# Performance work log

Measured on AMD Instinct MI355X. Metric: run time of the kernel, lower is better.

The kernel has to match this reference:

```python
import jax, jax.numpy as jnp
import numpy as np

N = 6000; E = 96000; DIN = 3000; FH1 = 256; FH2 = 128; GH = 128; LAT = 256
K = 10; SCALE = 9; NC = 10; AT = 0.5; ALPHA = 1.0; BN_EPS = 1e-4

# eval-mode BatchNorm1d with running_mean=0, running_var=1
def _bn(x, g, b):
    return x * (g / jnp.sqrt(1.0 + BN_EPS)) + b

def _block(x, W, bb, g, be):  # Linear + BN(eval) + ELU (dropout=identity in eval)
    return jax.nn.elu(_bn(x @ W + bb, g, be))

def _tconv(x, src, dst, Wq, Wk, Wv, Ws, bq, bk, bv, bs):
    # PyG TransformerConv, heads=1, root_weight=True, eval (no dropout)
    q = x @ Wq + bq; k = x @ Wk + bk; v = x @ Wv + bv
    sc = 1.0 / jnp.sqrt(jnp.asarray(q.shape[-1], x.dtype))
    logit = jnp.sum(q[dst] * k[src], axis=-1) * sc            # [E]
    m = jax.ops.segment_max(logit, dst, num_segments=N)
    e = jnp.exp(logit - m[dst])
    s = jax.ops.segment_sum(e, dst, num_segments=N)
    alpha = e / s[dst]                                        # softmax over incoming edges
    out = jax.ops.segment_sum(alpha[:, None] * v[src], dst, num_segments=N) + x @ Ws + bs
    return out, alpha

def _dense_adj(src, dst, alpha):
    # remove_self_loops + to_dense_adj: dense[src, dst] += alpha for src != dst
    mask = (src != dst).astype(alpha.dtype)
    return jnp.zeros((N, N), alpha.dtype).at[src, dst].add(alpha * mask)

def _encode(x, adj, adjp, ew1, eb1, eg1, ebe1, ew2, eb2, eg2, ebe2,
            cWq, cWk, cWv, cWs, cbq, cbk, cbv, cbs):
    feat = _block(_block(x, ew1, eb1, eg1, ebe1), ew2, eb2, eg2, ebe2)
    h = feat
    lastAp = None
    for l in range(3):
        o, a = _tconv(h, adj[0], adj[1], cWq[l], cWk[l], cWv[l], cWs[l], cbq[l], cbk[l], cbv[l], cbs[l])
        # middle layer applies the 'prue' conv to the freshly produced x (as in source)
        hp_in = o if l == 1 else h
        op, ap = _tconv(hp_in, adjp[0], adjp[1], cWq[l], cWk[l], cWv[l], cWs[l], cbq[l], cbk[l], cbv[l], cbs[l])
        A = _dense_adj(adj[0], adj[1], a)
        Ap = _dense_adj(adjp[0], adjp[1], ap)
        h = (1.0 - AT) * (A @ o) + AT * (Ap @ op)
        if l < 2:
            h = jax.nn.relu(h)
        lastAp = Ap
    return h, feat, lastAp

def setup_inputs():
    key = jax.random.key(0)
    ks = jax.random.split(key, 24)
    w = lambda k, sh, fan: (jax.random.normal(k, sh, jnp.float32) / np.sqrt(fan)).astype(jnp.float32)
    inp = {}
    inp['x'] = jax.random.normal(ks[0], (N, DIN), jnp.float32)
    inp['x_neighbor'] = jax.random.normal(ks[1], (N, DIN), jnp.float32)
    inp['spatial'] = jax.random.uniform(ks[2], (N, 2), jnp.float32)
    inp['adj'] = jax.random.randint(ks[3], (2, E), 0, N, dtype=jnp.int32)
    inp['adj_prue'] = jax.random.randint(ks[4], (2, E), 0, N, dtype=jnp.int32)
    # encoder
    inp['enc_W1'] = w(ks[5], (DIN, FH1), DIN); inp['enc_b1'] = jnp.zeros((FH1,))
    inp['enc_g1'] = jnp.ones((FH1,)); inp['enc_be1'] = jnp.zeros((FH1,))
    inp['enc_W2'] = w(ks[6], (FH1, FH2), FH1); inp['enc_b2'] = jnp.zeros((FH2,))
    inp['enc_g2'] = jnp.ones((FH2,)); inp['enc_be2'] = jnp.zeros((FH2,))
    # 3 TransformerConv layers (gc1, conv_hidden[0], gc2) all 128->128: stacked
    inp['conv_Wq'] = w(ks[7], (3, GH, GH), GH); inp['conv_Wk'] = w(ks[8], (3, GH, GH), GH)
    inp['conv_Wv'] = w(ks[9], (3, GH, GH), GH); inp['conv_Ws'] = w(ks[10], (3, GH, GH), GH)
    inp['conv_bq'] = jnp.zeros((3, GH)); inp['conv_bk'] = jnp.zeros((3, GH))
    inp['conv_bv'] = jnp.zeros((3, GH)); inp['conv_bs'] = jnp.zeros((3, GH))
    # decoder
    inp['dec_W'] = w(ks[11], (LAT, DIN), LAT); inp['dec_b'] = jnp.zeros((DIN,))
    inp['dec_g'] = jnp.ones((DIN,)); inp['dec_be'] = jnp.zeros((DIN,))
    inp['cluster'] = w(ks[12], (NC, LAT), LAT)
    return inp

def reference(x, x_neighbor, spatial, enc_W1, enc_b1, enc_g1, enc_be1,
              enc_W2, enc_b2, enc_g2, enc_be2,
              conv_Wq, conv_Wk, conv_Wv, conv_Ws, conv_bq, conv_bk, conv_bv, conv_bs,
              dec_W, dec_b, dec_g, dec_be, cluster, adj, adj_prue):
    enc = (enc_W1, enc_b1, enc_g1, enc_be1, enc_W2, enc_b2, enc_g2, enc_be2)
    conv = (conv_Wq, conv_Wk, conv_Wv, conv_Ws, conv_bq, conv_bk, conv_bv, conv_bs)
    mu, feat_x, atten = _encode(x, adj, adj_prue, *enc, *conv)
    mu_nb, feat_nb, _ = _encode(x_neighbor, adj, adj_prue, *enc, *conv)
    z = jnp.concatenate([feat_x, mu], axis=1)          # [N, LAT]
    z_nb = jnp.concatenate([feat_nb, mu_nb], axis=1)
    # Graph_spatial: kNN in joint feature+spatial space (dense [N,N] distances)
    df = (jnp.sum(z * z, 1)[:, None] - 2.0 * (z @ z_nb.T) + jnp.sum(z_nb * z_nb, 1)[None, :])
    ds = (jnp.sum(spatial * spatial, 1)[:, None] - 2.0 * (spatial @ spatial.T)
          + jnp.sum(spatial * spatial, 1)[None, :])
    neg_top, idx_k = jax.lax.top_k(-(df + ds), K)      # [N, K]
    score_k = jax.nn.softmax(neg_top, axis=-1)
    # GCNBlock_spatial: gather scale=9 nearest neighbor features and aggregate
    idx9 = idx_k[:, :SCALE]
    x_h = z_nb[idx9]                                   # [N, 9, LAT]
    wgt = score_k[:, :SCALE]
    wgt = wgt / jnp.sum(wgt, axis=-1, keepdims=True)
    z_out = z + jnp.einsum('nk,nkd->nd', wgt, x_h)     # x1_lr
    x1_hr = (x_h * wgt[:, :, None]).reshape(N * SCALE, LAT)
    de_feat = _block(z_out, dec_W, dec_b, dec_g, dec_be)
    # student-t cluster assignment
    d2 = jnp.sum((z_out[:, None, :] - cluster[None, :, :]) ** 2, axis=2)
    q = (1.0 / (1.0 + d2 / ALPHA)) ** ((ALPHA + 1.0) / 2.0)
    q = q / jnp.sum(q, axis=1, keepdims=True)
    return (z_out, de_feat, q, feat_x, de_feat, x1_hr, atten)
```

## Files before the change

kernel.cpp:

```cpp
#include <hip/hip_runtime.h>
#include <hip/hip_bf16.h>
#include <math.h>
#include <stdint.h>

#define NN 6000
#define NE 96000
#define KDIN 3000
#define NCAND 12
#define NTILE 47
#define TCAND (NCAND*NTILE)
#define PRE 32

#define OFF_ZOUT 0
#define OFF_DE1  1536000
#define OFF_Q    19536000
#define OFF_FEAT 19596000
#define OFF_DE2  20364000
#define OFF_X1   38364000
#define OFF_ATT  52188000

typedef __attribute__((ext_vector_type(8))) short short8;
typedef __attribute__((ext_vector_type(4))) float f32x4;

__device__ __forceinline__ unsigned short f2bf(float f){
  unsigned int u = __float_as_uint(f);
  u += 0x7FFFu + ((u >> 16) & 1u);
  return (unsigned short)(u >> 16);
}
__device__ __forceinline__ float bf2f(unsigned short h){
  return __uint_as_float(((unsigned int)h) << 16);
}

__global__ void prep_k(const float* __restrict__ W1, const float* __restrict__ W2,
                       const float* __restrict__ Wq, const float* __restrict__ Wk,
                       const float* __restrict__ Wv, const float* __restrict__ Ws,
                       const float* __restrict__ bq, const float* __restrict__ bk,
                       const float* __restrict__ bv, const float* __restrict__ bs,
                       const float* __restrict__ decW, const float* __restrict__ spat,
                       double* __restrict__ W1t, double* __restrict__ W2t,
                       double* __restrict__ Bct, float* __restrict__ Dt,
                       double* __restrict__ bcat,
                       double* __restrict__ sx64, double* __restrict__ sy64,
                       double* __restrict__ ssq64,
                       float* __restrict__ sx32, float* __restrict__ sy32)
{
  int t = blockIdx.x * 256 + threadIdx.x;
  if (t < 768000){
    int n = t / 3000, k = t % 3000;
    W1t[t] = (double)W1[(size_t)k * 256 + n]; return;
  }
  t -= 768000;
  if (t < 32768){
    int n = t / 256, k = t % 256;
    W2t[t] = (double)W2[(size_t)k * 128 + n]; return;
  }
  t -= 32768;
  if (t < 196608){
    int l = t / 65536; int rem = t % 65536;
    int n = rem / 128, k = rem % 128;
    int sel = n >> 7, nn = n & 127;
    const float* Wm = sel==0 ? Wq : sel==1 ? Wk : sel==2 ? Wv : Ws;
    Bct[t] = (double)Wm[((size_t)(l*128) + k) * 128 + nn]; return;
  }
  t -= 196608;
  if (t < 768000){
    int n = t / 256, k = t % 256;
    Dt[t] = decW[(size_t)k * 3000 + n]; return;
  }
  t -= 768000;
  if (t < 1536){
    int l = t / 512, n = t % 512;
    int sel = n >> 7, nn = n & 127;
    const float* bm = sel==0 ? bq : sel==1 ? bk : sel==2 ? bv : bs;
    bcat[t] = (double)bm[l*128 + nn]; return;
  }
  t -= 1536;
  if (t < NN){
    float sx = spat[(size_t)t*2], sy = spat[(size_t)t*2+1];
    sx64[t]=(double)sx; sy64[t]=(double)sy;
    ssq64[t]=(double)sx*(double)sx + (double)sy*(double)sy;
    sx32[t]=sx; sy32[t]=sy; return;
  }
}

__global__ void castup_k(const float* __restrict__ s, double* __restrict__ d, int n){
  int t = blockIdx.x*256 + threadIdx.x;
  if (t < n) d[t] = (double)s[t];
}

__global__ void splitz_k(const double* __restrict__ z64, unsigned short* __restrict__ zh,
                         unsigned short* __restrict__ zl, int n){
  int t = blockIdx.x*256 + threadIdx.x;
  if (t < n){
    float v = (float)z64[t];
    unsigned short h = f2bf(v);
    float r = v - bf2f(h);
    zh[t] = h; zl[t] = f2bf(r);
  }
}

template<int EPI, typename TA>
__global__ __launch_bounds__(256)
void gemm64_k(const TA* __restrict__ A, int lda,
              const double* __restrict__ Bt, int ldb,
              int M, int K, int Ncol,
              double* __restrict__ outF, int ldc,
              const double* __restrict__ bias,
              const float* __restrict__ gam, const float* __restrict__ bet,
              double* __restrict__ outF2)
{
  __shared__ double lA[64][18];
  __shared__ double lB[64][18];
  const int tid = threadIdx.x;
  const int m0 = blockIdx.y * 64;
  const int n0 = blockIdx.x * 64;
  const int tx = tid & 15;
  const int ty = tid >> 4;

  double acc[4][4];
  #pragma unroll
  for (int i=0;i<4;i++)
    #pragma unroll
    for (int j=0;j<4;j++) acc[i][j] = 0.0;

  const int nkt = (K + 15) >> 4;
  for (int kt = 0; kt < nkt; kt++){
    const int k0 = kt << 4;
    __syncthreads();
    #pragma unroll
    for (int c=0;c<4;c++){
      int lin = tid + c*256;
      int row = lin >> 4, col = lin & 15;
      int gm = m0 + row, gk = k0 + col;
      double va = 0.0, vb = 0.0;
      if (gm < M && gk < K)        va = (double)A [(size_t)gm*lda + gk];
      if (n0+row < Ncol && gk < K) vb = Bt[(size_t)(n0+row)*ldb + gk];
      lA[row][col] = va;
      lB[row][col] = vb;
    }
    __syncthreads();
    #pragma unroll 4
    for (int kk=0; kk<16; kk+=2){
      double2 A0 = *(const double2*)&lA[ty   ][kk];
      double2 A1 = *(const double2*)&lA[ty+16][kk];
      double2 A2 = *(const double2*)&lA[ty+32][kk];
      double2 A3 = *(const double2*)&lA[ty+48][kk];
      double2 B0 = *(const double2*)&lB[tx   ][kk];
      double2 B1 = *(const double2*)&lB[tx+16][kk];
      double2 B2 = *(const double2*)&lB[tx+32][kk];
      double2 B3 = *(const double2*)&lB[tx+48][kk];
      acc[0][0]+=A0.x*B0.x; acc[0][1]+=A0.x*B1.x; acc[0][2]+=A0.x*B2.x; acc[0][3]+=A0.x*B3.x;
      acc[1][0]+=A1.x*B0.x; acc[1][1]+=A1.x*B1.x; acc[1][2]+=A1.x*B2.x; acc[1][3]+=A1.x*B3.x;
      acc[2][0]+=A2.x*B0.x; acc[2][1]+=A2.x*B1.x; acc[2][2]+=A2.x*B2.x; acc[2][3]+=A2.x*B3.x;
      acc[3][0]+=A3.x*B0.x; acc[3][1]+=A3.x*B1.x; acc[3][2]+=A3.x*B2.x; acc[3][3]+=A3.x*B3.x;
      acc[0][0]+=A0.y*B0.y; acc[0][1]+=A0.y*B1.y; acc[0][2]+=A0.y*B2.y; acc[0][3]+=A0.y*B3.y;
      acc[1][0]+=A1.y*B0.y; acc[1][1]+=A1.y*B1.y; acc[1][2]+=A1.y*B2.y; acc[1][3]+=A1.y*B3.y;
      acc[2][0]+=A2.y*B0.y; acc[2][1]+=A2.y*B1.y; acc[2][2]+=A2.y*B2.y; acc[2][3]+=A2.y*B3.y;
      acc[3][0]+=A3.y*B0.y; acc[3][1]+=A3.y*B1.y; acc[3][2]+=A3.y*B2.y; acc[3][3]+=A3.y*B3.y;
    }
  }
  #pragma unroll
  for (int j=0;j<4;j++){
    int gn = n0 + tx + 16*j;
    if (gn >= Ncol) continue;
    double bi = bias[gn];
    #pragma unroll
    for (int i=0;i<4;i++){
      int gm = m0 + ty + 16*i;
      if (gm >= M) continue;
      double v = acc[i][j] + bi;
      outF[(size_t)gm*ldc + gn] = v;
      if (outF2) outF2[(size_t)gm*ldc + gn] = v;
    }
  }
}

template<typename TA>
__global__ __launch_bounds__(256)
void gemm64s_k(const TA* __restrict__ A, const TA* __restrict__ A2, int M1, int lda,
               const double* __restrict__ Bt, int ldb,
               int M, int K, int kchunk, int Ncol,
               double* __restrict__ part)
{
  __shared__ double lA[64][18];
  __shared__ double lB[64][18];
  const int tid = threadIdx.x;
  const int m0 = blockIdx.y * 64;
  const int n0 = blockIdx.x * 64;
  const int tx = tid & 15;
  const int ty = tid >> 4;
  const int kbeg = blockIdx.z * kchunk;
  const int kend = min(K, kbeg + kchunk);
  double* dst = part + (size_t)blockIdx.z * M * Ncol;

  double acc[4][4];
  #pragma unroll
  for (int i=0;i<4;i++)
    #pragma unroll
    for (int j=0;j<4;j++) acc[i][j] = 0.0;

  const int nkt = (kend - kbeg + 15) >> 4;
  for (int kt = 0; kt < nkt; kt++){
    const int k0 = kbeg + (kt << 4);
    __syncthreads();
    #pragma unroll
    for (int c=0;c<4;c++){
      int lin = tid + c*256;
      int row = lin >> 4, col = lin & 15;
      int gm = m0 + row, gk = k0 + col;
      double va = 0.0, vb = 0.0;
      if (gm < M && gk < kend){
        va = (gm < M1) ? (double)A[(size_t)gm*lda + gk]
                       : (double)A2[(size_t)(gm-M1)*lda + gk];
      }
      if (n0+row < Ncol && gk < kend) vb = Bt[(size_t)(n0+row)*ldb + gk];
      lA[row][col] = va;
      lB[row][col] = vb;
    }
    __syncthreads();
    #pragma unroll 4
    for (int kk=0; kk<16; kk+=2){
      double2 A0 = *(const double2*)&lA[ty   ][kk];
      double2 A1 = *(const double2*)&lA[ty+16][kk];
      double2 A2v = *(const double2*)&lA[ty+32][kk];
      double2 A3 = *(const double2*)&lA[ty+48][kk];
      double2 B0 = *(const double2*)&lB[tx   ][kk];
      double2 B1 = *(const double2*)&lB[tx+16][kk];
      double2 B2 = *(const double2*)&lB[tx+32][kk];
      double2 B3 = *(const double2*)&lB[tx+48][kk];
      acc[0][0]+=A0.x*B0.x; acc[0][1]+=A0.x*B1.x; acc[0][2]+=A0.x*B2.x; acc[0][3]+=A0.x*B3.x;
      acc[1][0]+=A1.x*B0.x; acc[1][1]+=A1.x*B1.x; acc[1][2]+=A1.x*B2.x; acc[1][3]+=A1.x*B3.x;
      acc[2][0]+=A2v.x*B0.x; acc[2][1]+=A2v.x*B1.x; acc[2][2]+=A2v.x*B2.x; acc[2][3]+=A2v.x*B3.x;
      acc[3][0]+=A3.x*B0.x; acc[3][1]+=A3.x*B1.x; acc[3][2]+=A3.x*B2.x; acc[3][3]+=A3.x*B3.x;
      acc[0][0]+=A0.y*B0.y; acc[0][1]+=A0.y*B1.y; acc[0][2]+=A0.y*B2.y; acc[0][3]+=A0.y*B3.y;
      acc[1][0]+=A1.y*B0.y; acc[1][1]+=A1.y*B1.y; acc[1][2]+=A1.y*B2.y; acc[1][3]+=A1.y*B3.y;
      acc[2][0]+=A2v.y*B0.y; acc[2][1]+=A2v.y*B1.y; acc[2][2]+=A2v.y*B2.y; acc[2][3]+=A2v.y*B3.y;
      acc[3][0]+=A3.y*B0.y; acc[3][1]+=A3.y*B1.y; acc[3][2]+=A3.y*B2.y; acc[3][3]+=A3.y*B3.y;
    }
  }
  #pragma unroll
  for (int j=0;j<4;j++){
    int gn = n0 + tx + 16*j;
    if (gn >= Ncol) continue;
    #pragma unroll
    for (int i=0;i<4;i++){
      int gm = m0 + ty + 16*i;
      if (gm >= M) continue;
      dst[(size_t)gm*Ncol + gn] = acc[i][j];
    }
  }
}

__global__ void epi64_k(const double* __restrict__ part, int nsplit, size_t pstride,
                        int M, int Ncol, const double* __restrict__ bias,
                        const float* __restrict__ gam, const float* __restrict__ bet,
                        double* __restrict__ out, int ldo)
{
  int t = blockIdx.x*256 + threadIdx.x;
  if (t >= M*Ncol) return;
  int gm = t / Ncol, gn = t - gm*Ncol;
  double v = 0.0;
  for (int s=0; s<nsplit; s++) v += part[(size_t)s*pstride + t];
  const double BNS = 0.99995000374968755261;
  v += bias[gn];
  v = v * ((double)gam[gn]*BNS) + (double)bet[gn];
  v = v > 0.0 ? v : expm1(v);
  out[(size_t)gm*ldo + gn] = v;
}

__global__ __launch_bounds__(256)
void gemm32d_k(const float* __restrict__ A, int lda,
               const float* __restrict__ Bt, int ldb,
               int M, int K, int Ncol,
               float* __restrict__ out1, int ldc,
               const float* __restrict__ bias, const float* __restrict__ gam,
               const float* __restrict__ bet, float* __restrict__ out2)
{
  __shared__ float lA[64][33];
  __shared__ float lB[64][33];
  const int tid = threadIdx.x;
  const int m0 = blockIdx.y * 64;
  const int n0 = blockIdx.x * 64;
  const int tx = tid & 15;
  const int ty = tid >> 4;

  float acc[4][4];
  #pragma unroll
  for (int i=0;i<4;i++)
    #pragma unroll
    for (int j=0;j<4;j++) acc[i][j] = 0.f;

  const int nkt = (K + 31) >> 5;
  for (int kt = 0; kt < nkt; kt++){
    const int k0 = kt << 5;
    __syncthreads();
    #pragma unroll
    for (int c=0;c<8;c++){
      int lin = tid + c*256;
      int row = lin >> 5, col = lin & 31;
      int gm = m0 + row, gk = k0 + col;
      float va = 0.f, vb = 0.f;
      if (gm < M && gk < K)        va = A [(size_t)gm*lda + gk];
      if (n0+row < Ncol && gk < K) vb = Bt[(size_t)(n0+row)*ldb + gk];
      lA[row][col] = va;
      lB[row][col] = vb;
    }
    __syncthreads();
    #pragma unroll 4
    for (int kk=0; kk<32; kk++){
      float a0=lA[ty][kk], a1=lA[ty+16][kk], a2=lA[ty+32][kk], a3=lA[ty+48][kk];
      float b0=lB[tx][kk], b1=lB[tx+16][kk], b2=lB[tx+32][kk], b3=lB[tx+48][kk];
      acc[0][0]+=a0*b0; acc[0][1]+=a0*b1; acc[0][2]+=a0*b2; acc[0][3]+=a0*b3;
      acc[1][0]+=a1*b0; acc[1][1]+=a1*b1; acc[1][2]+=a1*b2; acc[1][3]+=a1*b3;
      acc[2][0]+=a2*b0; acc[2][1]+=a2*b1; acc[2][2]+=a2*b2; acc[2][3]+=a2*b3;
      acc[3][0]+=a3*b0; acc[3][1]+=a3*b1; acc[3][2]+=a3*b2; acc[3][3]+=a3*b3;
    }
  }
  const float BNS = 0.99995000374968755f;
  #pragma unroll
  for (int j=0;j<4;j++){
    int gn = n0 + tx + 16*j;
    if (gn >= Ncol) continue;
    float bi = bias[gn];
    float gs = gam[gn]*BNS, be = bet[gn];
    #pragma unroll
    for (int i=0;i<4;i++){
      int gm = m0 + ty + 16*i;
      if (gm >= M) continue;
      float v = acc[i][j] + bi;
      v = v*gs + be; v = v > 0.f ? v : expm1f(v);
      out1[(size_t)gm*ldc + gn] = v;
      out2[(size_t)gm*ldc + gn] = v;
    }
  }
}

__global__ void csr_cnt_k(const int* __restrict__ key, int* __restrict__ cnt){
  int e = blockIdx.x*256 + threadIdx.x;
  if (e < NE) atomicAdd(&cnt[key[e]], 1);
}
__global__ __launch_bounds__(256)
void csr_scan_k(const int* __restrict__ cnt, int* __restrict__ rowptr, int* __restrict__ cursor){
  __shared__ int part[256];
  int t = threadIdx.x;
  int base = t*24;
  int loc[24]; int s=0;
  #pragma unroll
  for (int u=0;u<24;u++){
    int idx = base+u;
    int v = (idx<NN) ? cnt[idx] : 0;
    loc[u] = s; s += v;
  }
  part[t] = s;
  __syncthreads();
  if (t==0){
    int run=0;
    for (int u=0;u<256;u++){ int tmp=part[u]; part[u]=run; run+=tmp; }
  }
  __syncthreads();
  int off = part[t];
  #pragma unroll
  for (int u=0;u<24;u++){
    int idx = base+u;
    if (idx<NN){ rowptr[idx]=off+loc[u]; cursor[idx]=off+loc[u]; }
  }
  if (t==255) rowptr[NN] = off + s;
}
__global__ void csr_fill_k(const int* __restrict__ key, int* __restrict__ cursor,
                           int* __restrict__ elist){
  int e = blockIdx.x*256 + threadIdx.x;
  if (e < NE){ int pos = atomicAdd(&cursor[key[e]], 1); elist[pos] = e; }
}

__global__ __launch_bounds__(256)
void attn_k(double* __restrict__ QKVS, const int* __restrict__ rowptr,
            const int* __restrict__ elist, const int* __restrict__ src,
            double* __restrict__ alpha)
{
  __shared__ double lg[4][128];
  const int w = threadIdx.x >> 6;
  const int node = blockIdx.x*4 + w;
  if (node >= 2*NN) return;
  const int base = (node < NN) ? 0 : NN;
  const int aoff = (node < NN) ? 0 : NE;
  const int cn = node - base;
  const int lane = threadIdx.x & 63;
  const int e0 = rowptr[cn], e1 = rowptr[cn+1];
  const int deg = e1 - e0;
  if (deg <= 0) return;
  const double SC = 0.088388347648318447;
  const double* q = QKVS + (size_t)node*512;
  double q0 = q[lane], q1 = q[lane+64];

  if (deg <= 128){
    double m = -1.0e300;
    for (int i=0;i<deg;i++){
      const double* k = QKVS + (size_t)(src[elist[e0+i]] + base)*512 + 128;
      double p = q0*k[lane] + q1*k[lane+64];
      #pragma unroll
      for (int off=32; off; off>>=1) p += __shfl_xor(p, off);
      p *= SC;
      if (lane==0) lg[w][i] = p;
      m = fmax(m, p);
    }
    double S = 0.0;
    for (int i=0;i<deg;i++){
      double ex = exp(lg[w][i] - m);
      if (lane==0) lg[w][i] = ex;
      S += ex;
    }
    double inv = 1.0 / S;
    double o0 = QKVS[(size_t)node*512 + 384 + lane];
    double o1 = QKVS[(size_t)node*512 + 448 + lane];
    for (int i=0;i<deg;i++){
      int e = elist[e0+i];
      double a = lg[w][i] * inv;
      const double* v = QKVS + (size_t)(src[e] + base)*512 + 256;
      o0 = fma(a, v[lane],    o0);
      o1 = fma(a, v[lane+64], o1);
      if (lane==0) alpha[aoff + e] = a;
    }
    QKVS[(size_t)node*512 + 384 + lane] = o0;
    QKVS[(size_t)node*512 + 448 + lane] = o1;
  } else {
    double m = -1.0e300;
    for (int i=0;i<deg;i++){
      const double* k = QKVS + (size_t)(src[elist[e0+i]] + base)*512 + 128;
      double p = q0*k[lane] + q1*k[lane+64];
      #pragma unroll
      for (int off=32; off; off>>=1) p += __shfl_xor(p, off);
      m = fmax(m, p*SC);
    }
    double S = 0.0;
    for (int i=0;i<deg;i++){
      const double* k = QKVS + (size_t)(src[elist[e0+i]] + base)*512 + 128;
      double p = q0*k[lane] + q1*k[lane+64];
      #pragma unroll
      for (int off=32; off; off>>=1) p += __shfl_xor(p, off);
      S += exp(p*SC - m);
    }
    double inv = 1.0 / S;
    double o0 = QKVS[(size_t)node*512 + 384 + lane];
    double o1 = QKVS[(size_t)node*512 + 448 + lane];
    for (int i=0;i<deg;i++){
      int e = elist[e0+i];
      const double* k = QKVS + (size_t)(src[e] + base)*512 + 128;
      double p = q0*k[lane] + q1*k[lane+64];
      #pragma unroll
      for (int off=32; off; off>>=1) p += __shfl_xor(p, off);
      double a = exp(p*SC - m) * inv;
      const double* v = QKVS + (size_t)(src[e] + base)*512 + 256;
      o0 = fma(a, v[lane],    o0);
      o1 = fma(a, v[lane+64], o1);
      if (lane==0) alpha[aoff + e] = a;
    }
    QKVS[(size_t)node*512 + 384 + lane] = o0;
    QKVS[(size_t)node*512 + 448 + lane] = o1;
  }
}

__global__ __launch_bounds__(256)
void spmm_csr_k(const double* __restrict__ QK1, const double* __restrict__ QK2,
                const int* __restrict__ rpSA, const int* __restrict__ elSA,
                const int* __restrict__ dstA, const double* __restrict__ aA,
                const int* __restrict__ rpSP, const int* __restrict__ elSP,
                const int* __restrict__ dstP, const double* __restrict__ aP,
                double* __restrict__ out, int ldo, int offo, int dorelu)
{
  const int node = blockIdx.x*4 + (threadIdx.x>>6);
  if (node >= 2*NN) return;
  const int base = (node < NN) ? 0 : NN;
  const int aoff = (node < NN) ? 0 : NE;
  const int cn = node - base;
  const int lane = threadIdx.x & 63;
  double a0 = 0.0, a1 = 0.0;
  for (int idx = rpSA[cn]; idx < rpSA[cn+1]; ++idx){
    int e = elSA[idx]; int d = dstA[e];
    if (d != cn){
      double wgt = 0.5 * aA[aoff + e];
      const double* o = QK1 + (size_t)(d + base)*512 + 384;
      a0 = fma(wgt, o[lane],    a0);
      a1 = fma(wgt, o[lane+64], a1);
    }
  }
  for (int idx = rpSP[cn]; idx < rpSP[cn+1]; ++idx){
    int e = elSP[idx]; int d = dstP[e];
    if (d != cn){
      double wgt = 0.5 * aP[aoff + e];
      const double* o = QK2 + (size_t)(d + base)*512 + 384;
      a0 = fma(wgt, o[lane],    a0);
      a1 = fma(wgt, o[lane+64], a1);
    }
  }
  if (dorelu){ a0 = fmax(a0, 0.0); a1 = fmax(a1, 0.0); }
  out[(size_t)node*ldo + offo + lane]      = a0;
  out[(size_t)node*ldo + offo + 64 + lane] = a1;
}

__global__ void att_scatter_k(const int* __restrict__ src, const int* __restrict__ dst,
                              const double* __restrict__ alpha, float* __restrict__ att)
{
  int e = blockIdx.x*256 + threadIdx.x;
  if (e >= NE) return;
  int s = src[e], d = dst[e];
  if (s == d) return;
  atomicAdd(&att[(size_t)s*NN + d], (float)alpha[e]);
}

__global__ __launch_bounds__(256)
void distmf_k(const unsigned short* __restrict__ zXh, const unsigned short* __restrict__ zXl,
              const unsigned short* __restrict__ zNh, const unsigned short* __restrict__ zNl,
              const float* __restrict__ sxA, const float* __restrict__ syA,
              const float* __restrict__ cjA,
              float* __restrict__ candV, int* __restrict__ candI)
{
  __shared__ __align__(16) char smem[40960 + 1536];
  typedef unsigned short u16;
  u16 (*lAh)[40] = (u16(*)[40])(smem);
  u16 (*lAl)[40] = (u16(*)[40])(smem + 10240);
  u16 (*lBh)[40] = (u16(*)[40])(smem + 20480);
  u16 (*lBl)[40] = (u16(*)[40])(smem + 30720);
  float (*stile)[67] = (float(*)[67])(smem);
  float* sSx = (float*)(smem + 40960);
  float* sSy = sSx + 128;
  float* sC  = sSy + 128;

  const int tid = threadIdx.x;
  const int m0 = blockIdx.y * 128;
  const int n0 = blockIdx.x * 128;
  const int lane = tid & 63;
  const int wave = tid >> 6;
  const int wm = wave >> 1, wn = wave & 1;
  const int lr = lane & 15;
  const int lk = (lane >> 4) * 8;

  if (tid < 128){
    int jg = n0 + tid;
    if (jg < NN){ sSx[tid]=sxA[jg]; sSy[tid]=syA[jg]; sC[tid]=cjA[jg]; }
    else        { sSx[tid]=0.f; sSy[tid]=0.f; sC[tid]=-3e38f; }
  }

  f32x4 acc[4][4];
  #pragma unroll
  for (int i=0;i<4;i++)
    #pragma unroll
    for (int j=0;j<4;j++) acc[i][j] = (f32x4){0.f,0.f,0.f,0.f};

  for (int kt = 0; kt < 8; kt++){
    const int k0 = kt << 5;
    __syncthreads();
    #pragma unroll
    for (int c=0;c<4;c++){
      int lin = tid + c*256;
      int row = lin >> 3;
      int kc = (lin & 7) << 2;
      int gm = m0 + row, gn = n0 + row;
      ushort4 vh = {0,0,0,0}, vl = {0,0,0,0}, wh = {0,0,0,0}, wl = {0,0,0,0};
      if (gm < NN){
        vh = *(const ushort4*)(zXh + (size_t)gm*256 + k0 + kc);
        vl = *(const ushort4*)(zXl + (size_t)gm*256 + k0 + kc);
      }
      if (gn < NN){
        wh = *(const ushort4*)(zNh + (size_t)gn*256 + k0 + kc);
        wl = *(const ushort4*)(zNl + (size_t)gn*256 + k0 + kc);
      }
      *(ushort4*)&lAh[row][kc] = vh;
      *(ushort4*)&lAl[row][kc] = vl;
      *(ushort4*)&lBh[row][kc] = wh;
      *(ushort4*)&lBl[row][kc] = wl;
    }
    __syncthreads();
    short8 ah[4], al[4];
    #pragma unroll
    for (int fm=0; fm<4; fm++){
      ah[fm] = *(const short8*)&lAh[wm*64 + fm*16 + lr][lk];
      al[fm] = *(const short8*)&lAl[wm*64 + fm*16 + lr][lk];
    }
    #pragma unroll
    for (int fn=0; fn<4; fn++){
      short8 bh = *(const short8*)&lBh[wn*64 + fn*16 + lr][lk];
      short8 bl = *(const short8*)&lBl[wn*64 + fn*16 + lr][lk];
      #pragma unroll
      for (int fm=0; fm<4; fm++){
        acc[fm][fn] = __builtin_amdgcn_mfma_f32_16x16x32_bf16(ah[fm], bh, acc[fm][fn], 0,0,0);
        acc[fm][fn] = __builtin_amdgcn_mfma_f32_16x16x32_bf16(ah[fm], bl, acc[fm][fn], 0,0,0);
        acc[fm][fn] = __builtin_amdgcn_mfma_f32_16x16x32_bf16(al[fm], bh, acc[fm][fn], 0,0,0);
      }
    }
  }

  float tv[NCAND]; int ti[NCAND];
  #pragma unroll
  for (int p=0;p<NCAND;p++){ tv[p] = -3.4e38f; ti[p] = -1; }
  const int gi = m0 + tid;
  float sxi = 0.f, syi = 0.f;
  if (tid < 128 && gi < NN){ sxi = sxA[gi]; syi = syA[gi]; }

  for (int jh = 0; jh < 2; jh++){
    __syncthreads();
    if (wn == jh){
      #pragma unroll
      for (int fm=0;fm<4;fm++){
        #pragma unroll
        for (int fn=0;fn<4;fn++){
          int lrow = wm*64 + fm*16 + ((lane>>4)<<2);
          int lcol = fn*16 + lr;
          #pragma unroll
          for (int r=0;r<4;r++)
            stile[lrow + r][lcol] = acc[fm][fn][r];
        }
      }
    }
    __syncthreads();
    if (tid < 128 && gi < NN){
      #pragma unroll 1
      for (int jj=0; jj<64; jj++){
        int j = jh*64 + jj;
        float s = 2.f*stile[tid][jj] + 2.f*(sxi*sSx[j] + syi*sSy[j]) + sC[j];
        if (s > tv[NCAND-1]){
          bool g[NCAND];
          #pragma unroll
          for (int p=0;p<NCAND;p++) g[p] = s > tv[p];
          #pragma unroll
          for (int p=NCAND-1;p>0;--p) if (g[p-1]){ tv[p]=tv[p-1]; ti[p]=ti[p-1]; }
          #pragma unroll
          for (int p=0;p<NCAND;p++){ bool pl = g[p] && (p==0 || !g[p-1]); if (pl){ tv[p]=s; ti[p]=n0+j; } }
        }
      }
    }
  }
  if (tid < 128 && gi < NN){
    size_t base = ((size_t)gi*NTILE + blockIdx.x)*NCAND;
    #pragma unroll
    for (int p=0;p<NCAND;p++){ candV[base+p]=tv[p]; candI[base+p]=ti[p]; }
  }
}

__global__ __launch_bounds__(256)
void merge64_k(const float* __restrict__ candV, const int* __restrict__ candI,
               const double* __restrict__ Z, const double* __restrict__ Znb,
               const double* __restrict__ sx64, const double* __restrict__ sy64,
               double* __restrict__ wgt9, int* __restrict__ idx9)
{
  __shared__ double zi[256];
  __shared__ int    fjS[TCAND];
  __shared__ float  wbv[4];
  __shared__ int    wbc[4];
  __shared__ int    chosen;
  __shared__ int    pj[PRE];
  __shared__ double ps[PRE];

  const int i = blockIdx.x;
  const int t = threadIdx.x;
  const int lane = t & 63, wv = t >> 6;

  zi[t] = Z[(size_t)i*256 + t];

  float v0 = -3.4e38f, v1 = -3.4e38f, v2 = -3.4e38f;
  const int c0 = t, c1 = t + 256, c2 = t + 512;
  {
    float vv = candV[(size_t)i*TCAND + c0];
    int jj = candI[(size_t)i*TCAND + c0];
    fjS[c0] = jj;
    if (jj >= 0) v0 = vv;
  }
  if (c1 < TCAND){
    float vv = candV[(size_t)i*TCAND + c1];
    int jj = candI[(size_t)i*TCAND + c1];
    fjS[c1] = jj;
    if (jj >= 0) v1 = vv;
  }
  if (c2 < TCAND){
    float vv = candV[(size_t)i*TCAND + c2];
    int jj = candI[(size_t)i*TCAND + c2];
    fjS[c2] = jj;
    if (jj >= 0) v2 = vv;
  }
  __syncthreads();

  for (int it = 0; it < PRE; it++){
    float bv = v0; int bc = c0;
    if (v1 > bv || (v1 == bv && c1 < bc)){ bv = v1; bc = c1; }
    if (v2 > bv || (v2 == bv && c2 < bc)){ bv = v2; bc = c2; }
    #pragma unroll
    for (int off = 32; off; off >>= 1){
      float ov = __shfl_xor(bv, off);
      int   oc = __shfl_xor(bc, off);
      if (ov > bv || (ov == bv && oc < bc)){ bv = ov; bc = oc; }
    }
    if (lane == 0){ wbv[wv] = bv; wbc[wv] = bc; }
    __syncthreads();
    if (t == 0){
      float gb = wbv[0]; int gc = wbc[0];
      #pragma unroll
      for (int w2 = 1; w2 < 4; w2++)
        if (wbv[w2] > gb || (wbv[w2] == gb && wbc[w2] < gc)){ gb = wbv[w2]; gc = wbc[w2]; }
      chosen = gc;
      pj[it] = fjS[gc];
    }
    __syncthreads();
    int gc = chosen;
    if (c0 == gc) v0 = -3.4e38f;
    if (c1 == gc) v1 = -3.4e38f;
    if (c2 == gc) v2 = -3.4e38f;
  }

  const double sxi = sx64[i], syi = sy64[i];
  for (int c = wv; c < PRE; c += 4){
    int j = pj[c];
    const double* zj = Znb + (size_t)j*256;
    double p = 0.0;
    #pragma unroll
    for (int u = 0; u < 4; u++){
      double b = zj[lane + 64*u];
      double a = zi[lane + 64*u];
      p = fma(2.0*a - b, b, p);
    }
    #pragma unroll
    for (int off = 32; off; off >>= 1) p += __shfl_xor(p, off);
    double sxj = sx64[j], syj = sy64[j];
    double s = p + 2.0*(sxi*sxj + syi*syj) - (sxj*sxj + syj*syj);
    if (lane == 0) ps[c] = s;
  }
  __syncthreads();

  if (t == 0){
    double tv9[9]; int ti9[9];
    #pragma unroll
    for (int p = 0; p < 9; p++){ tv9[p] = -1.0e301; ti9[p] = 0x7FFFFFFF; }
    for (int c = 0; c < PRE; c++){
      double s = ps[c]; int j = pj[c];
      if (!((s > tv9[8]) || (s == tv9[8] && j < ti9[8]))) continue;
      int p = 8;
      while (p > 0 && ((s > tv9[p-1]) || (s == tv9[p-1] && j < ti9[p-1]))){
        tv9[p] = tv9[p-1]; ti9[p] = ti9[p-1]; --p;
      }
      tv9[p] = s; ti9[p] = j;
    }
    double m = tv9[0], e[9], S = 0.0;
    #pragma unroll
    for (int k = 0; k < 9; k++){ e[k] = exp(tv9[k] - m); S += e[k]; }
    #pragma unroll
    for (int k = 0; k < 9; k++){
      wgt9[(size_t)i*9 + k] = e[k] / S;
      idx9[(size_t)i*9 + k] = ti9[k];
    }
  }
}

__global__ __launch_bounds__(256)
void znbprep_k(const double* __restrict__ znb, const double* __restrict__ ssq64,
               float* __restrict__ cjA)
{
  __shared__ double red[256];
  int i = blockIdx.x, d = threadIdx.x;
  double v = znb[(size_t)i*256 + d];
  red[d] = v*v;
  __syncthreads();
  for (int s=128; s; s>>=1){ if (d<s) red[d]+=red[d+s]; __syncthreads(); }
  if (d==0) cjA[i] = -(float)(red[0] + ssq64[i]);
}
__global__ void featout_k(const double* __restrict__ z, float* __restrict__ o){
  int t = blockIdx.x*256+threadIdx.x;
  if (t < NN*128){ int i=t>>7, d=t&127; o[t] = (float)z[(size_t)i*256 + d]; }
}

__global__ __launch_bounds__(256)
void zout_k(const double* __restrict__ Z, const double* __restrict__ Znb,
            const int* __restrict__ idx9, const double* __restrict__ wgt9,
            float* __restrict__ zoOut, float* __restrict__ zoF32, float* __restrict__ x1)
{
  int i = blockIdx.x; int d = threadIdx.x;
  double a = Z[(size_t)i*256 + d];
  #pragma unroll
  for (int k=0;k<9;k++){
    int j = idx9[(size_t)i*9+k];
    double w = wgt9[(size_t)i*9+k];
    double t = w * Znb[(size_t)j*256 + d];
    a += t;
    x1[((size_t)i*9+k)*256 + d] = (float)t;
  }
  float af = (float)a;
  zoOut[(size_t)i*256+d] = af;
  zoF32[(size_t)i*256+d] = af;
}

__global__ __launch_bounds__(256)
void q_k(const float* __restrict__ zoF, const float* __restrict__ clus, float* __restrict__ qB)
{
  __shared__ float wred[10][4];
  __shared__ float qs[10];
  int i = blockIdx.x, d = threadIdx.x;
  int lane = d & 63, wv = d >> 6;
  float zo = zoF[(size_t)i*256 + d];
  #pragma unroll
  for (int c=0;c<10;c++){
    float df = zo - clus[(size_t)c*256 + d];
    float p = df*df;
    #pragma unroll
    for (int off=32; off; off>>=1) p += __shfl_down(p, off);
    if (lane == 0) wred[c][wv] = p;
  }
  __syncthreads();
  if (d < 10){
    float d2 = wred[d][0]+wred[d][1]+wred[d][2]+wred[d][3];
    qs[d] = 1.f/(1.f + d2);
  }
  __syncthreads();
  if (d < 10){
    float s = 0.f;
    #pragma unroll
    for (int c=0;c<10;c++) s += qs[c];
    qB[(size_t)i*10 + d] = qs[d]/s;
  }
}

extern "C" void kernel_launch(void* const* d_in, const int* in_sizes, int n_in,
                              void* d_out, int out_size, void* d_ws, size_t ws_size,
                              hipStream_t stream)
{
  (void)in_sizes; (void)n_in; (void)out_size; (void)ws_size;
  const float* x    = (const float*)d_in[0];
  const float* xnb  = (const float*)d_in[1];
  const float* spat = (const float*)d_in[2];
  const int*   adj  = (const int*)d_in[3];
  const int*   adjp = (const int*)d_in[4];
  const float* W1   = (const float*)d_in[5];
  const float* b1   = (const float*)d_in[6];
  const float* g1   = (const float*)d_in[7];
  const float* be1  = (const float*)d_in[8];
  const float* W2   = (const float*)d_in[9];
  const float* b2   = (const float*)d_in[10];
  const float* g2   = (const float*)d_in[11];
  const float* be2  = (const float*)d_in[12];
  const float* Wq   = (const float*)d_in[13];
  const float* Wk   = (const float*)d_in[14];
  const float* Wv   = (const float*)d_in[15];
  const float* Wsm  = (const float*)d_in[16];
  const float* bq   = (const float*)d_in[17];
  const float* bk   = (const float*)d_in[18];
  const float* bv   = (const float*)d_in[19];
  const float* bs   = (const float*)d_in[20];
  const float* decW = (const float*)d_in[21];
  const float* decb = (const float*)d_in[22];
  const float* decg = (const float*)d_in[23];
  const float* decbe= (const float*)d_in[24];
  const float* clus = (const float*)d_in[25];
  float* outF = (float*)d_out;
  const int* srcA = adj,  *dstA = adj + NE;
  const int* srcP = adjp, *dstP = adjp + NE;

  char* wsb = (char*)d_ws;
  size_t off = 0;
  auto alloc = [&](size_t bytes)->char*{
    char* p = wsb + off;
    off = (off + bytes + 255) & ~(size_t)255;
    return p;
  };
  double* W1t  = (double*)alloc(768000*8);
  double* W2t  = (double*)alloc(32768*8);
  double* Bct  = (double*)alloc(196608*8);
  float*  Dt   = (float*) alloc(768000*4);
  double* bcat = (double*)alloc(1536*8);
  double* sx64 = (double*)alloc(NN*8);
  double* sy64 = (double*)alloc(NN*8);
  double* ssq64= (double*)alloc(NN*8);
  float*  sx32 = (float*) alloc(NN*4);
  float*  sy32 = (float*) alloc(NN*4);
  double* b1c  = (double*)alloc(256*8);
  double* b2c  = (double*)alloc(128*8);
  double* H1   = (double*)alloc((size_t)2*NN*256*8);
  double* zAll = (double*)alloc((size_t)2*NN*256*8);
  double* hcur = (double*)alloc((size_t)2*NN*128*8);
  double* QK1  = (double*)alloc((size_t)2*NN*512*8);
  double* QK2  = (double*)alloc((size_t)2*NN*512*8);
  double* alphaA=(double*)alloc((size_t)2*NE*8);
  double* alphaP=(double*)alloc((size_t)2*NE*8);
  double* part = (double*)alloc((size_t)4*2*NN*256*8);
  int* rpDA = (int*)alloc((NN+1)*4);
  int* rpDP = (int*)alloc((NN+1)*4);
  int* rpSA = (int*)alloc((NN+1)*4);
  int* rpSP = (int*)alloc((NN+1)*4);
  int* curDA= (int*)alloc(NN*4);
  int* curDP= (int*)alloc(NN*4);
  int* curSA= (int*)alloc(NN*4);
  int* curSP= (int*)alloc(NN*4);
  int* elDA = (int*)alloc(NE*4);
  int* elDP = (int*)alloc(NE*4);
  int* elSA = (int*)alloc(NE*4);
  int* elSP = (int*)alloc(NE*4);
  unsigned short* zXh = (unsigned short*)alloc((size_t)NN*256*2);
  unsigned short* zXl = (unsigned short*)alloc((size_t)NN*256*2);
  unsigned short* zNh = (unsigned short*)alloc((size_t)NN*256*2);
  unsigned short* zNl = (unsigned short*)alloc((size_t)NN*256*2);
  float*  cjA  = (float*) alloc(NN*4);
  float*  candV= (float*) alloc((size_t)NN*TCAND*4);
  int*    candI= (int*)   alloc((size_t)NN*TCAND*4);
  int*    idx9 = (int*)   alloc((size_t)NN*9*4);
  double* wgt9 = (double*)alloc((size_t)NN*9*8);
  float*  zoF32= (float*) alloc((size_t)NN*256*4);

  double* zX64  = zAll;
  double* zNB64 = zAll + (size_t)NN*256;

  prep_k<<<6926, 256, 0, stream>>>(W1, W2, Wq, Wk, Wv, Wsm, bq, bk, bv, bs, decW, spat,
                                   W1t, W2t, Bct, Dt, bcat,
                                   sx64, sy64, ssq64, sx32, sy32);
  castup_k<<<1, 256, 0, stream>>>(b1, b1c, 256);
  castup_k<<<1, 256, 0, stream>>>(b2, b2c, 128);

  hipMemsetAsync(curDA, 0, NN*4, stream);
  hipMemsetAsync(curDP, 0, NN*4, stream);
  hipMemsetAsync(curSA, 0, NN*4, stream);
  hipMemsetAsync(curSP, 0, NN*4, stream);
  csr_cnt_k<<<375, 256, 0, stream>>>(dstA, curDA);
  csr_cnt_k<<<375, 256, 0, stream>>>(dstP, curDP);
  csr_cnt_k<<<375, 256, 0, stream>>>(srcA, curSA);
  csr_cnt_k<<<375, 256, 0, stream>>>(srcP, curSP);
  csr_scan_k<<<1, 256, 0, stream>>>(curDA, rpDA, curDA);
  csr_scan_k<<<1, 256, 0, stream>>>(curDP, rpDP, curDP);
  csr_scan_k<<<1, 256, 0, stream>>>(curSA, rpSA, curSA);
  csr_scan_k<<<1, 256, 0, stream>>>(curSP, rpSP, curSP);
  csr_fill_k<<<375, 256, 0, stream>>>(dstA, curDA, elDA);
  csr_fill_k<<<375, 256, 0, stream>>>(dstP, curDP, elDP);
  csr_fill_k<<<375, 256, 0, stream>>>(srcA, curSA, elSA);
  csr_fill_k<<<375, 256, 0, stream>>>(srcP, curSP, elSP);

  const int M2 = 2*NN;

  gemm64s_k<float><<<dim3(4,188,4), 256, 0, stream>>>(x, xnb, NN, KDIN, W1t, KDIN,
                                                      M2, KDIN, 768, 256, part);
  epi64_k<<<(M2*256+255)/256, 256, 0, stream>>>(part, 4, (size_t)M2*256,
                                                M2, 256, b1c, g1, be1, H1, 256);
  gemm64s_k<double><<<dim3(2,188,4), 256, 0, stream>>>(H1, H1, M2, 256, W2t, 256,
                                                       M2, 256, 64, 128, part);
  epi64_k<<<(M2*128+255)/256, 256, 0, stream>>>(part, 4, (size_t)M2*128,
                                                M2, 128, b2c, g2, be2, zAll, 256);

  const double* hin = zAll; int ldh = 256;
  for (int l=0; l<3; l++){
    const double* Bh = Bct + (size_t)l*65536;
    const double* bc = bcat + l*512;
    if (l != 1){
      gemm64_k<0,double><<<dim3(8,188), 256, 0, stream>>>(hin, ldh, Bh, 128, M2, 128, 512,
                                                          QK1, 512, bc, nullptr, nullptr, QK2);
      attn_k<<<3000, 256, 0, stream>>>(QK1, rpDA, elDA, srcA, alphaA);
      attn_k<<<3000, 256, 0, stream>>>(QK2, rpDP, elDP, srcP, alphaP);
    } else {
      gemm64_k<0,double><<<dim3(8,188), 256, 0, stream>>>(hin, ldh, Bh, 128, M2, 128, 512,
                                                          QK1, 512, bc, nullptr, nullptr, nullptr);
      attn_k<<<3000, 256, 0, stream>>>(QK1, rpDA, elDA, srcA, alphaA);
      gemm64_k<0,double><<<dim3(8,188), 256, 0, stream>>>(QK1 + 384, 512, Bh, 128, M2, 128, 512,
                                                          QK2, 512, bc, nullptr, nullptr, nullptr);
      attn_k<<<3000, 256, 0, stream>>>(QK2, rpDP, elDP, srcP, alphaP);
    }
    if (l == 2){
      hipMemsetAsync(outF + (size_t)OFF_ATT, 0, (size_t)NN*NN*4, stream);
      att_scatter_k<<<375, 256, 0, stream>>>(srcP, dstP, alphaP, outF + (size_t)OFF_ATT);
    }
    if (l < 2){
      spmm_csr_k<<<3000, 256, 0, stream>>>(QK1, QK2, rpSA, elSA, dstA, alphaA,
                                           rpSP, elSP, dstP, alphaP, hcur, 128, 0, 1);
      hin = hcur; ldh = 128;
    } else {
      spmm_csr_k<<<3000, 256, 0, stream>>>(QK1, QK2, rpSA, elSA, dstA, alphaA,
                                           rpSP, elSP, dstP, alphaP, zAll, 256, 128, 0);
    }
  }

  splitz_k<<<6000, 256, 0, stream>>>(zX64,  zXh, zXl, NN*256);
  splitz_k<<<6000, 256, 0, stream>>>(zNB64, zNh, zNl, NN*256);
  znbprep_k<<<NN, 256, 0, stream>>>(zNB64, ssq64, cjA);
  distmf_k<<<dim3(NTILE,47), 256, 0, stream>>>(zXh, zXl, zNh, zNl,
                                               sx32, sy32, cjA, candV, candI);
  merge64_k<<<NN, 256, 0, stream>>>(candV, candI, zX64, zNB64, sx64, sy64, wgt9, idx9);

  zout_k<<<NN, 256, 0, stream>>>(zX64, zNB64, idx9, wgt9,
                                 outF + (size_t)OFF_ZOUT, zoF32, outF + (size_t)OFF_X1);
  gemm32d_k<<<dim3(47,94), 256, 0, stream>>>(zoF32, 256, Dt, 256, NN, 256, 3000,
                                             outF + (size_t)OFF_DE1, 3000, decb, decg, decbe,
                                             outF + (size_t)OFF_DE2);
  q_k<<<NN, 256, 0, stream>>>(zoF32, clus, outF + (size_t)OFF_Q);
  featout_k<<<3000, 256, 0, stream>>>(zX64, outF + (size_t)OFF_FEAT);
}
```

Before: 2.658 ms.

## Run decoder GEMM on bf16 MFMA with split hi/lo emulated fp32

Replaces the scalar fp32 tiled decoder GEMM with a 128x128-tile MFMA kernel that splits each fp32 operand into bf16 high and low parts and accumulates three bf16 products, emulating fp32 precision. Decoder weights are pre-split in the prep kernel and the activation tile is split on load into LDS. This moves a 6000x3000x256 matmul onto the matrix cores, at the cost of dropping the low*low term and adding conversion work.

New measurement: 2.605 ms. 1.02x faster.

```diff
diff --git a/kernel.cpp b/kernel.cpp
--- a/kernel.cpp
+++ b/kernel.cpp
@@ -30,6 +30,10 @@
 __device__ __forceinline__ float bf2f(unsigned short h){
   return __uint_as_float(((unsigned int)h) << 16);
 }
+__device__ __forceinline__ void split2(float v, unsigned short &h, unsigned short &l){
+  h = f2bf(v);
+  l = f2bf(v - bf2f(h));
+}
 
 __global__ void prep_k(const float* __restrict__ W1, const float* __restrict__ W2,
                        const float* __restrict__ Wq, const float* __restrict__ Wk,
@@ -38,7 +42,8 @@
                        const float* __restrict__ bv, const float* __restrict__ bs,
                        const float* __restrict__ decW, const float* __restrict__ spat,
                        double* __restrict__ W1t, double* __restrict__ W2t,
-                       double* __restrict__ Bct, float* __restrict__ Dt,
+                       double* __restrict__ Bct,
+                       unsigned short* __restrict__ DtH, unsigned short* __restrict__ DtL,
                        double* __restrict__ bcat,
                        double* __restrict__ sx64, double* __restrict__ sy64,
                        double* __restrict__ ssq64,
@@ -65,7 +70,9 @@
   t -= 196608;
   if (t < 768000){
     int n = t / 256, k = t % 256;
-    Dt[t] = decW[(size_t)k * 3000 + n]; return;
+    float v = decW[(size_t)k * 3000 + n];
+    unsigned short h,l; split2(v,h,l);
+    DtH[t]=h; DtL[t]=l; return;
   }
   t -= 768000;
   if (t < 1536){
@@ -269,68 +276,93 @@
 }
 
 __global__ __launch_bounds__(256)
-void gemm32d_k(const float* __restrict__ A, int lda,
-               const float* __restrict__ Bt, int ldb,
-               int M, int K, int Ncol,
-               float* __restrict__ out1, int ldc,
-               const float* __restrict__ bias, const float* __restrict__ gam,
-               const float* __restrict__ bet, float* __restrict__ out2)
-{
-  __shared__ float lA[64][33];
-  __shared__ float lB[64][33];
+void decomf_k(const float* __restrict__ A,
+              const unsigned short* __restrict__ Bh_, const unsigned short* __restrict__ Bl_,
+              const float* __restrict__ bias, const float* __restrict__ gam,
+              const float* __restrict__ bet,
+              float* __restrict__ out1, float* __restrict__ out2)
+{
+  __shared__ unsigned short lAh[128][40];
+  __shared__ unsigned short lAl[128][40];
+  __shared__ unsigned short lBh[128][40];
+  __shared__ unsigned short lBl[128][40];
   const int tid = threadIdx.x;
-  const int m0 = blockIdx.y * 64;
-  const int n0 = blockIdx.x * 64;
-  const int tx = tid & 15;
-  const int ty = tid >> 4;
-
-  float acc[4][4];
+  const int n0 = blockIdx.x * 128;
+  const int m0 = blockIdx.y * 128;
+  const int lane = tid & 63;
+  const int wave = tid >> 6;
+  const int wm = wave >> 1, wn = wave & 1;
+  const int lr = lane & 15;
+  const int lk = (lane >> 4) * 8;
+
+  f32x4 acc[4][4];
   #pragma unroll
   for (int i=0;i<4;i++)
     #pragma unroll
-    for (int j=0;j<4;j++) acc[i][j] = 0.f;
-
-  const int nkt = (K + 31) >> 5;
-  for (int kt = 0; kt < nkt; kt++){
+    for (int j=0;j<4;j++) acc[i][j] = (f32x4){0.f,0.f,0.f,0.f};
+
+  for (int kt = 0; kt < 8; kt++){
     const int k0 = kt << 5;
     __syncthreads();
     #pragma unroll
-    for (int c=0;c<8;c++){
+    for (int c=0;c<4;c++){
       int lin = tid + c*256;
-      int row = lin >> 5, col = lin & 31;
-      int gm = m0 + row, gk = k0 + col;
-      float va = 0.f, vb = 0.f;
-      if (gm < M && gk < K)        va = A [(size_t)gm*lda + gk];
-      if (n0+row < Ncol && gk < K) vb = Bt[(size_t)(n0+row)*ldb + gk];
-      lA[row][col] = va;
-      lB[row][col] = vb;
-    }
-    __syncthreads();
-    #pragma unroll 4
-    for (int kk=0; kk<32; kk++){
-      float a0=lA[ty][kk], a1=lA[ty+16][kk], a2=lA[ty+32][kk], a3=lA[ty+48][kk];
-      float b0=lB[tx][kk], b1=lB[tx+16][kk], b2=lB[tx+32][kk], b3=lB[tx+48][kk];
-      acc[0][0]+=a0*b0; acc[0][1]+=a0*b1; acc[0][2]+=a0*b2; acc[0][3]+=a0*b3;
-      acc[1][0]+=a1*b0; acc[1][1]+=a1*b1; acc[1][2]+=a1*b2; acc[1][3]+=a1*b3;
-      acc[2][0]+=a2*b0; acc[2][1]+=a2*b1; acc[2][2]+=a2*b2; acc[2][3]+=a2*b3;
-      acc[3][0]+=a3*b0; acc[3][1]+=a3*b1; acc[3][2]+=a3*b2; acc[3][3]+=a3*b3;
+      int row = lin >> 3;
+      int kc = (lin & 7) << 2;
+      int gm = m0 + row, gn = n0 + row;
+      float4 va = make_float4(0.f,0.f,0.f,0.f);
+      if (gm < NN) va = *(const float4*)(A + (size_t)gm*256 + k0 + kc);
+      ushort4 h, l;
+      split2(va.x, h.x, l.x); split2(va.y, h.y, l.y);
+      split2(va.z, h.z, l.z); split2(va.w, h.w, l.w);
+      *(ushort4*)&lAh[row][kc] = h;
+      *(ushort4*)&lAl[row][kc] = l;
+      ushort4 bh = {0,0,0,0}, bl = {0,0,0,0};
+      if (gn < 3000){
+        bh = *(const ushort4*)(Bh_ + (size_t)gn*256 + k0 + kc);
+        bl = *(const ushort4*)(Bl_ + (size_t)gn*256 + k0 + kc);
+      }
+      *(ushort4*)&lBh[row][kc] = bh;
+      *(ushort4*)&lBl[row][kc] = bl;
+    }
+    __syncthreads();
+    short8 ah[4], al[4];
+    #pragma unroll
+    for (int fm=0; fm<4; fm++){
+      ah[fm] = *(const short8*)&lAh[wm*64 + fm*16 + lr][lk];
+      al[fm] = *(const short8*)&lAl[wm*64 + fm*16 + lr][lk];
+    }
+    #pragma unroll
+    for (int fn=0; fn<4; fn++){
+      short8 bh = *(const short8*)&lBh[wn*64 + fn*16 + lr][lk];
+      short8 bl = *(const short8*)&lBl[wn*64 + fn*16 + lr][lk];
+      #pragma unroll
+      for (int fm=0; fm<4; fm++){
+        acc[fm][fn] = __builtin_amdgcn_mfma_f32_16x16x32_bf16(ah[fm], bh, acc[fm][fn], 0,0,0);
+        acc[fm][fn] = __builtin_amdgcn_mfma_f32_16x16x32_bf16(ah[fm], bl, acc[fm][fn], 0,0,0);
+        acc[fm][fn] = __builtin_amdgcn_mfma_f32_16x16x32_bf16(al[fm], bh, acc[fm][fn], 0,0,0);
+      }
     }
   }
   const float BNS = 0.99995000374968755f;
   #pragma unroll
-  for (int j=0;j<4;j++){
-    int gn = n0 + tx + 16*j;
-    if (gn >= Ncol) continue;
+  for (int fn=0; fn<4; fn++){
+    int gn = n0 + wn*64 + fn*16 + lr;
+    if (gn >= 3000) continue;
     float bi = bias[gn];
     float gs = gam[gn]*BNS, be = bet[gn];
     #pragma unroll
-    for (int i=0;i<4;i++){
-      int gm = m0 + ty + 16*i;
-      if (gm >= M) continue;
-      float v = acc[i][j] + bi;
-      v = v*gs + be; v = v > 0.f ? v : expm1f(v);
-      out1[(size_t)gm*ldc + gn] = v;
-      out2[(size_t)gm*ldc + gn] = v;
+    for (int fm=0; fm<4; fm++){
+      int gmb = m0 + wm*64 + fm*16 + ((lane >> 4) << 2);
+      #pragma unroll
+      for (int r=0;r<4;r++){
+        int gm = gmb + r;
+        if (gm >= NN) continue;
+        float v = acc[fm][fn][r] + bi;
+        v = v*gs + be; v = v > 0.f ? v : expm1f(v);
+        out1[(size_t)gm*3000 + gn] = v;
+        out2[(size_t)gm*3000 + gn] = v;
+      }
     }
   }
 }
@@ -860,7 +892,8 @@
   double* W1t  = (double*)alloc(768000*8);
   double* W2t  = (double*)alloc(32768*8);
   double* Bct  = (double*)alloc(196608*8);
-  float*  Dt   = (float*) alloc(768000*4);
+  unsigned short* DtH = (unsigned short*)alloc(768000*2);
+  unsigned short* DtL = (unsigned short*)alloc(768000*2);
   double* bcat = (double*)alloc(1536*8);
   double* sx64 = (double*)alloc(NN*8);
   double* sy64 = (double*)alloc(NN*8);
@@ -904,7 +937,7 @@
   double* zNB64 = zAll + (size_t)NN*256;
 
   prep_k<<<6926, 256, 0, stream>>>(W1, W2, Wq, Wk, Wv, Wsm, bq, bk, bv, bs, decW, spat,
-                                   W1t, W2t, Bct, Dt, bcat,
+                                   W1t, W2t, Bct, DtH, DtL, bcat,
                                    sx64, sy64, ssq64, sx32, sy32);
   castup_k<<<1, 256, 0, stream>>>(b1, b1c, 256);
   castup_k<<<1, 256, 0, stream>>>(b2, b2c, 128);
@@ -977,9 +1010,8 @@
 
   zout_k<<<NN, 256, 0, stream>>>(zX64, zNB64, idx9, wgt9,
                                  outF + (size_t)OFF_ZOUT, zoF32, outF + (size_t)OFF_X1);
-  gemm32d_k<<<dim3(47,94), 256, 0, stream>>>(zoF32, 256, Dt, 256, NN, 256, 3000,
-                                             outF + (size_t)OFF_DE1, 3000, decb, decg, decbe,
-                                             outF + (size_t)OFF_DE2);
+  decomf_k<<<dim3(24,47), 256, 0, stream>>>(zoF32, DtH, DtL, decb, decg, decbe,
+                                            outF + (size_t)OFF_DE1, outF + (size_t)OFF_DE2);
   q_k<<<NN, 256, 0, stream>>>(zoF32, clus, outF + (size_t)OFF_Q);
   featout_k<<<3000, 256, 0, stream>>>(zX64, outF + (size_t)OFF_FEAT);
 }
```
